# Kernel optimization log

Measured on AMD Instinct MI355X. Metric: run time of the kernel, lower is better.

Reference implementation:

```python
import jax, jax.numpy as jnp
import numpy as np

N, V, E = 65536, 2048, 1024
TEMPERATURE = 0.5
EPS = 1e-10
LOG_PARAM_Q = -2.995732273553991


def _l2_normalize(x, axis):
    # matches torch F.normalize(p=2): x / max(||x||, 1e-12)
    n = jnp.sqrt(jnp.sum(x * x, axis=axis, keepdims=True))
    return x / jnp.maximum(n, 1e-12)


def setup_inputs() -> dict:
    key = jax.random.key(0)
    k1, k2, k3 = jax.random.split(key, 3)
    z = jax.random.normal(k1, (N, E), dtype=jnp.float32)
    emb_weight = jax.random.normal(k2, (V, E), dtype=jnp.float32)
    U = jax.random.uniform(k3, (N, V), dtype=jnp.float32)
    return {"z": z, "emb_weight": emb_weight, "U": U}


def reference(z, emb_weight, U):
    kappa_q = jnp.exp(jnp.float32(LOG_PARAM_Q)) + jnp.float32(1.0)
    zn = _l2_normalize(z, axis=1)              # [N, E]
    emb = _l2_normalize(emb_weight, axis=1)    # [V, E]
    # logit = -distances = kappa_q * z @ emb.T
    logit = kappa_q * jnp.matmul(zn, emb.T)    # [N, V]
    # gumbel-softmax sample (training branch)
    g = -jnp.log(-jnp.log(U + EPS) + EPS)
    tokens = jax.nn.softmax((logit + g) / TEMPERATURE, axis=-1)  # [N, V]
    z_q = jnp.matmul(tokens, emb)              # [N, E]
    return (tokens, z_q)
```

## Files before the change

kernel.cpp:

```cpp
#include <hip/hip_runtime.h>
#include <hip/hip_bf16.h>
#include <stdint.h>

typedef short bf16x8 __attribute__((ext_vector_type(8)));
typedef float floatx4 __attribute__((ext_vector_type(4)));

#define N_ROWS 65536
#define V_DIM 2048
#define E_DIM 1024

__device__ __forceinline__ short f2bf(float x) {
  union { float f; uint32_t u; } c; c.f = x;
  uint32_t r = (c.u + 0x7FFFu + ((c.u >> 16) & 1u)) >> 16;
  return (short)(uint16_t)r;
}
__device__ __forceinline__ float bf16f(short b) {
  union { uint32_t u; float f; } c; c.u = ((uint32_t)(uint16_t)b) << 16;
  return c.f;
}

__device__ __forceinline__ float wave_sum(float v) {
#pragma unroll
  for (int o = 32; o > 0; o >>= 1) v += __shfl_xor(v, o);
  return v;
}
__device__ __forceinline__ float wave_max(float v) {
#pragma unroll
  for (int o = 32; o > 0; o >>= 1) v = fmaxf(v, __shfl_xor(v, o));
  return v;
}

__device__ __forceinline__ void gll16(const short* g, short* l) {
  __builtin_amdgcn_global_load_lds(
      (const __attribute__((address_space(1))) void*)g,
      (__attribute__((address_space(3))) void*)l, 16, 0, 0);
}

#define FRAG(base, R, c) \
  (*(const bf16x8*)((const char*)(base) + ((R) << 7) + (((((c) >> 3) ^ ((R) & 7))) << 4)))

__global__ __launch_bounds__(256) void k_norm_emb(const float* __restrict__ W,
                                                  short* __restrict__ embn,
                                                  short* __restrict__ embnT) {
  const int v = blockIdx.x;
  const int t = threadIdx.x;
  const int w = t >> 6, l = t & 63;
  const float4 val = *(const float4*)&W[(size_t)v * E_DIM + t * 4];
  float ss = val.x * val.x + val.y * val.y + val.z * val.z + val.w * val.w;
  ss = wave_sum(ss);
  __shared__ float red[4];
  if (l == 0) red[w] = ss;
  __syncthreads();
  ss = red[0] + red[1] + red[2] + red[3];
  const float inv = 1.0f / fmaxf(sqrtf(ss), 1e-12f);
  short4 o;
  o.x = f2bf(val.x * inv);
  o.y = f2bf(val.y * inv);
  o.z = f2bf(val.z * inv);
  o.w = f2bf(val.w * inv);
  *(short4*)&embn[(size_t)v * E_DIM + t * 4] = o;
  embnT[(size_t)(t * 4 + 0) * V_DIM + v] = o.x;
  embnT[(size_t)(t * 4 + 1) * V_DIM + v] = o.y;
  embnT[(size_t)(t * 4 + 2) * V_DIM + v] = o.z;
  embnT[(size_t)(t * 4 + 3) * V_DIM + v] = o.w;
}

__global__ __launch_bounds__(256) void k_norm_z(const float* __restrict__ Z,
                                                short* __restrict__ zn) {
  const int w = threadIdx.x >> 6, l = threadIdx.x & 63;
  const int row = blockIdx.x * 4 + w;
  const float* zr = Z + (size_t)row * E_DIM;
  float4 v[4];
  float ss = 0.f;
#pragma unroll
  for (int i = 0; i < 4; ++i) {
    v[i] = *(const float4*)&zr[(i * 64 + l) * 4];
    ss += v[i].x * v[i].x + v[i].y * v[i].y + v[i].z * v[i].z + v[i].w * v[i].w;
  }
  ss = wave_sum(ss);
  const float SCALE = 2.0f * (expf(-2.995732273553991f) + 1.0f);
  const float inv = SCALE / fmaxf(sqrtf(ss), 1e-12f);
  short* zo = zn + (size_t)row * E_DIM;
#pragma unroll
  for (int i = 0; i < 4; ++i) {
    short4 o;
    o.x = f2bf(v[i].x * inv);
    o.y = f2bf(v[i].y * inv);
    o.z = f2bf(v[i].z * inv);
    o.w = f2bf(v[i].w * inv);
    *(short4*)&zo[(i * 64 + l) * 4] = o;
  }
}

template <int KDIM, int NBX, int EPI>
__global__ __launch_bounds__(512, 2) void k_gemm8(
    const short* __restrict__ A, const short* __restrict__ B,
    const float* __restrict__ U, short* __restrict__ Pb,
    float* __restrict__ partials, const float* __restrict__ invsum,
    float* __restrict__ C, int cpx) {
  __shared__ __align__(16) short Sm[65536];
  const int NT = KDIM / 32;
  const int tid = threadIdx.x;
  const int wv = tid >> 6, lane = tid & 63;
  const int lr = lane & 15, lh = lane >> 4;
  const int wr = wv >> 2, wc = wv & 3;
  const int d = blockIdx.x;
  const int L = (d & 7) * cpx + (d >> 3);
  const int by = L / NBX, bx = L % NBX;
  const int m0 = by * 256, n0 = bx * 256;
  const int sg = (((lane & 3) ^ ((lane >> 2) & 3) ^ ((lane >> 4) & 3)) << 3);
  const int srow = wv * 16 + (lane >> 2);
  const short* gA = A + (size_t)(m0 + srow) * KDIM + sg;
  const short* gB = B + (size_t)(n0 + srow) * KDIM + sg;
  const int fslot = lh ^ ((lr ^ (lr >> 2)) & 3);
  const int aoff = wr * 8192 + lr * 64 + fslot * 16;
  const int boff = wc * 4096 + lr * 64 + fslot * 16;

#pragma unroll
  for (int t = 0; t < 2; ++t) {
#pragma unroll
    for (int q = 0; q < 2; ++q) {
      gll16(gA + (size_t)(q * 128) * KDIM + t * 32, Sm + t * 8192 + q * 4096 + wv * 512);
      gll16(gB + (size_t)(q * 128) * KDIM + t * 32, Sm + 32768 + t * 8192 + q * 4096 + wv * 512);
    }
  }
  asm volatile("s_waitcnt vmcnt(4)" ::: "memory");
  __builtin_amdgcn_s_barrier();
  __builtin_amdgcn_sched_barrier(0);

  floatx4 acc[8][4] = {};

#define DO_TILE(KT, STAGE)                                                          \
  {                                                                                 \
    const int cb_ = (KT) & 3;                                                       \
    const char* Ab_ = (const char*)Sm + cb_ * 16384;                                \
    const char* Bb_ = (const char*)Sm + 65536 + cb_ * 16384;                        \
    short* An_ = Sm + (((KT) + 2) & 3) * 8192;                                      \
    short* Bn_ = Sm + 32768 + (((KT) + 2) & 3) * 8192;                              \
    const size_t kc_ = (size_t)((KT) + 2) * 32;                                     \
    bf16x8 bfr[4], af[4];                                                           \
    _Pragma("unroll")                                                               \
    for (int n = 0; n < 4; ++n) bfr[n] = *(const bf16x8*)(Bb_ + boff + n * 1024);   \
    _Pragma("unroll")                                                               \
    for (int i = 0; i < 4; ++i) af[i] = *(const bf16x8*)(Ab_ + aoff + i * 1024);    \
    if (STAGE) {                                                                    \
      _Pragma("unroll")                                                             \
      for (int q = 0; q < 2; ++q) {                                                 \
        gll16(gA + (size_t)(q * 128) * KDIM + kc_, An_ + q * 4096 + wv * 512);      \
        gll16(gB + (size_t)(q * 128) * KDIM + kc_, Bn_ + q * 4096 + wv * 512);      \
      }                                                                             \
    }                                                                               \
    __builtin_amdgcn_s_setprio(1);                                                  \
    _Pragma("unroll")                                                               \
    for (int i = 0; i < 4; ++i) {                                                   \
      _Pragma("unroll")                                                             \
      for (int n = 0; n < 4; ++n)                                                   \
        acc[i][n] =                                                                 \
            __builtin_amdgcn_mfma_f32_16x16x32_bf16(af[i], bfr[n], acc[i][n], 0, 0, 0); \
    }                                                                               \
    __builtin_amdgcn_s_setprio(0);                                                  \
    _Pragma("unroll")                                                               \
    for (int i = 0; i < 4; ++i)                                                     \
      af[i] = *(const bf16x8*)(Ab_ + aoff + 4096 + i * 1024);                       \
    __builtin_amdgcn_s_setprio(1);                                                  \
    _Pragma("unroll")                                                               \
    for (int i = 0; i < 4; ++i) {                                                   \
      _Pragma("unroll")                                                             \
      for (int n = 0; n < 4; ++n)                                                   \
        acc[4 + i][n] =                                                             \
            __builtin_amdgcn_mfma_f32_16x16x32_bf16(af[i], bfr[n], acc[4 + i][n], 0, 0, 0); \
    }                                                                               \
    __builtin_amdgcn_s_setprio(0);                                                  \
    if (STAGE) { asm volatile("s_waitcnt vmcnt(4)" ::: "memory"); }                 \
    else       { asm volatile("s_waitcnt vmcnt(0)" ::: "memory"); }                 \
    __builtin_amdgcn_s_barrier();                                                   \
    __builtin_amdgcn_sched_barrier(0);                                              \
  }

  for (int kt = 0; kt < NT - 2; ++kt) DO_TILE(kt, 1);
  DO_TILE(NT - 2, 0);
  DO_TILE(NT - 1, 0);
#undef DO_TILE

  const int gr0 = m0 + wr * 128 + lh * 4;
  const int gc0 = n0 + wc * 64 + lr;
  if (EPI == 0) {
    float rs[8][4] = {};
#pragma unroll
    for (int m = 0; m < 8; ++m)
#pragma unroll
      for (int n = 0; n < 4; ++n) {
        const int col = gc0 + n * 16;
#pragma unroll
        for (int j = 0; j < 4; ++j) {
          const int row = gr0 + m * 16 + j;
          const size_t idx = (size_t)row * V_DIM + col;
          const float u = U[idx];
          const float e = __expf(acc[m][n][j] - 2.f * __logf(-__logf(u + 1e-10f) + 1e-10f));
          const short eb = f2bf(e);
          Pb[idx] = eb;
          rs[m][j] += bf16f(eb);
        }
      }
#pragma unroll
    for (int m = 0; m < 8; ++m)
#pragma unroll
      for (int j = 0; j < 4; ++j) {
        float s = rs[m][j];
        s += __shfl_xor(s, 1); s += __shfl_xor(s, 2);
        s += __shfl_xor(s, 4); s += __shfl_xor(s, 8);
        if (lr == 0)
          partials[(size_t)(gr0 + m * 16 + j) * 32 + bx * 4 + wc] = s;
      }
  } else {
#pragma unroll
    for (int m = 0; m < 8; ++m)
#pragma unroll
      for (int j = 0; j < 4; ++j) {
        const int row = gr0 + m * 16 + j;
        const float s = invsum[row];
#pragma unroll
        for (int n = 0; n < 4; ++n)
          C[(size_t)row * E_DIM + gc0 + n * 16] = acc[m][n][j] * s;
      }
  }
}

__global__ __launch_bounds__(256) void k_rowsum_inv(const float* __restrict__ partials,
                                                    float* __restrict__ invsum) {
  const int r = blockIdx.x * 256 + threadIdx.x;
  const float4* p = (const float4*)&partials[(size_t)r * 32];
  float s = 0.f;
#pragma unroll
  for (int i = 0; i < 8; ++i) { float4 v = p[i]; s += v.x + v.y + v.z + v.w; }
  invsum[r] = 1.f / s;
}

__global__ __launch_bounds__(256) void k_token_norm(const short* __restrict__ Pb,
                                                    const float* __restrict__ invsum,
                                                    float* __restrict__ tokens) {
  const size_t stride = (size_t)gridDim.x * 256 * 8;
  for (size_t i = ((size_t)blockIdx.x * 256 + threadIdx.x) * 8;
       i < (size_t)N_ROWS * V_DIM; i += stride) {
    const float s = invsum[i >> 11];
    const bf16x8 v = *(const bf16x8*)&Pb[i];
    float4 o0, o1;
    o0.x = bf16f(v[0]) * s; o0.y = bf16f(v[1]) * s;
    o0.z = bf16f(v[2]) * s; o0.w = bf16f(v[3]) * s;
    o1.x = bf16f(v[4]) * s; o1.y = bf16f(v[5]) * s;
    o1.z = bf16f(v[6]) * s; o1.w = bf16f(v[7]) * s;
    *(float4*)&tokens[i] = o0;
    *(float4*)&tokens[i + 4] = o1;
  }
}

__global__ __launch_bounds__(256) void k_gemm_nt(const short* __restrict__ A,
                                                 const short* __restrict__ B,
                                                 float* __restrict__ C,
                                                 int lda, int ldb, int ldc, int K) {
  __shared__ __align__(16) short As[128][64];
  __shared__ __align__(16) short Bs[128][64];
  const int t = threadIdx.x;
  const int w = t >> 6, l = t & 63;
  const int lr = l & 15, lh = l >> 4;
  const int m0 = blockIdx.y * 128, n0 = blockIdx.x * 128;
  const int wm = (w >> 1) * 64, wn = (w & 1) * 64;
  floatx4 acc[4][4] = {};
  for (int k0 = 0; k0 < K; k0 += 64) {
    __syncthreads();
#pragma unroll
    for (int i = 0; i < 4; ++i) {
      const int c = i * 256 + t;
      const int r = c >> 3, c8 = (c & 7) * 8;
      *(bf16x8*)&As[r][c8] = *(const bf16x8*)&A[(size_t)(m0 + r) * lda + k0 + c8];
      *(bf16x8*)&Bs[r][c8] = *(const bf16x8*)&B[(size_t)(n0 + r) * ldb + k0 + c8];
    }
    __syncthreads();
#pragma unroll
    for (int kk = 0; kk < 64; kk += 32) {
      bf16x8 af[4], bfr[4];
#pragma unroll
      for (int m = 0; m < 4; ++m) af[m] = *(const bf16x8*)&As[wm + m * 16 + lr][kk + lh * 8];
#pragma unroll
      for (int n = 0; n < 4; ++n) bfr[n] = *(const bf16x8*)&Bs[wn + n * 16 + lr][kk + lh * 8];
#pragma unroll
      for (int m = 0; m < 4; ++m)
#pragma unroll
        for (int n = 0; n < 4; ++n)
          acc[m][n] = __builtin_amdgcn_mfma_f32_16x16x32_bf16(af[m], bfr[n], acc[m][n], 0, 0, 0);
    }
  }
#pragma unroll
  for (int m = 0; m < 4; ++m)
#pragma unroll
    for (int n = 0; n < 4; ++n) {
      const int col = n0 + wn + n * 16 + lr;
#pragma unroll
      for (int j = 0; j < 4; ++j)
        C[(size_t)(m0 + wm + m * 16 + lh * 4 + j) * ldc + col] = acc[m][n][j];
    }
}

__global__ __launch_bounds__(256) void k_gemm_nt_f32a(const float* __restrict__ A,
                                                      const short* __restrict__ B,
                                                      float* __restrict__ C,
                                                      int lda, int ldb, int ldc, int K) {
  __shared__ __align__(16) short As[128][64];
  __shared__ __align__(16) short Bs[128][64];
  const int t = threadIdx.x;
  const int w = t >> 6, l = t & 63;
  const int lr = l & 15, lh = l >> 4;
  const int m0 = blockIdx.y * 128, n0 = blockIdx.x * 128;
  const int wm = (w >> 1) * 64, wn = (w & 1) * 64;
  floatx4 acc[4][4] = {};
  for (int k0 = 0; k0 < K; k0 += 64) {
    __syncthreads();
#pragma unroll
    for (int i = 0; i < 4; ++i) {
      const int c = i * 256 + t;
      const int r = c >> 3, c8 = (c & 7) * 8;
      const float4 a0 = *(const float4*)&A[(size_t)(m0 + r) * lda + k0 + c8];
      const float4 a1 = *(const float4*)&A[(size_t)(m0 + r) * lda + k0 + c8 + 4];
      bf16x8 va;
      va[0] = f2bf(a0.x); va[1] = f2bf(a0.y); va[2] = f2bf(a0.z); va[3] = f2bf(a0.w);
      va[4] = f2bf(a1.x); va[5] = f2bf(a1.y); va[6] = f2bf(a1.z); va[7] = f2bf(a1.w);
      *(bf16x8*)&As[r][c8] = va;
      *(bf16x8*)&Bs[r][c8] = *(const bf16x8*)&B[(size_t)(n0 + r) * ldb + k0 + c8];
    }
    __syncthreads();
#pragma unroll
    for (int kk = 0; kk < 64; kk += 32) {
      bf16x8 af[4], bfr[4];
#pragma unroll
      for (int m = 0; m < 4; ++m) af[m] = *(const bf16x8*)&As[wm + m * 16 + lr][kk + lh * 8];
#pragma unroll
      for (int n = 0; n < 4; ++n) bfr[n] = *(const bf16x8*)&Bs[wn + n * 16 + lr][kk + lh * 8];
#pragma unroll
      for (int m = 0; m < 4; ++m)
#pragma unroll
        for (int n = 0; n < 4; ++n)
          acc[m][n] = __builtin_amdgcn_mfma_f32_16x16x32_bf16(af[m], bfr[n], acc[m][n], 0, 0, 0);
    }
  }
#pragma unroll
  for (int m = 0; m < 4; ++m)
#pragma unroll
    for (int n = 0; n < 4; ++n) {
      const int col = n0 + wn + n * 16 + lr;
#pragma unroll
      for (int j = 0; j < 4; ++j)
        C[(size_t)(m0 + wm + m * 16 + lh * 4 + j) * ldc + col] = acc[m][n][j];
    }
}

__global__ __launch_bounds__(256) void k_gumbel_softmax(float* __restrict__ S,
                                                        const float* __restrict__ U) {
  const int t = threadIdx.x;
  const int w = t >> 6, l = t & 63;
  const size_t base = (size_t)blockIdx.x * V_DIM + t * 8;
  const float4 s0 = *(const float4*)&S[base];
  const float4 s1 = *(const float4*)&S[base + 4];
  const float4 u0 = *(const float4*)&U[base];
  const float4 u1 = *(const float4*)&U[base + 4];
  float x[8];
  x[0] = s0.x - 2.f * __logf(-__logf(u0.x + 1e-10f) + 1e-10f);
  x[1] = s0.y - 2.f * __logf(-__logf(u0.y + 1e-10f) + 1e-10f);
  x[2] = s0.z - 2.f * __logf(-__logf(u0.z + 1e-10f) + 1e-10f);
  x[3] = s0.w - 2.f * __logf(-__logf(u0.w + 1e-10f) + 1e-10f);
  x[4] = s1.x - 2.f * __logf(-__logf(u1.x + 1e-10f) + 1e-10f);
  x[5] = s1.y - 2.f * __logf(-__logf(u1.y + 1e-10f) + 1e-10f);
  x[6] = s1.z - 2.f * __logf(-__logf(u1.z + 1e-10f) + 1e-10f);
  x[7] = s1.w - 2.f * __logf(-__logf(u1.w + 1e-10f) + 1e-10f);
  float lm = x[0];
#pragma unroll
  for (int i = 1; i < 8; ++i) lm = fmaxf(lm, x[i]);
  lm = wave_max(lm);
  __shared__ float redA[4], redB[4];
  if (l == 0) redA[w] = lm;
  __syncthreads();
  const float m = fmaxf(fmaxf(redA[0], redA[1]), fmaxf(redA[2], redA[3]));
  float p[8];
  float ls = 0.f;
#pragma unroll
  for (int i = 0; i < 8; ++i) { p[i] = __expf(x[i] - m); ls += p[i]; }
  ls = wave_sum(ls);
  if (l == 0) redB[w] = ls;
  __syncthreads();
  const float inv = 1.0f / (redB[0] + redB[1] + redB[2] + redB[3]);
  float4 o0 = make_float4(p[0] * inv, p[1] * inv, p[2] * inv, p[3] * inv);
  float4 o1 = make_float4(p[4] * inv, p[5] * inv, p[6] * inv, p[7] * inv);
  *(float4*)&S[base] = o0;
  *(float4*)&S[base + 4] = o1;
}

extern "C" void kernel_launch(void* const* d_in, const int* in_sizes, int n_in,
                              void* d_out, int out_size, void* d_ws, size_t ws_size,
                              hipStream_t stream) {
  const float* z = (const float*)d_in[0];
  const float* W = (const float*)d_in[1];
  const float* U = (const float*)d_in[2];
  float* tokens = (float*)d_out;
  float* zq = tokens + (size_t)N_ROWS * V_DIM;
  short* zn = (short*)zq;

  short* embn = (short*)d_ws;
  short* embnT = embn + (size_t)V_DIM * E_DIM;

  const size_t NEED = (size_t)V_DIM * E_DIM * 2 * 2
                    + (size_t)N_ROWS * 32 * 4
                    + (size_t)N_ROWS * 4
                    + (size_t)N_ROWS * V_DIM * 2;

  k_norm_emb<<<V_DIM, 256, 0, stream>>>(W, embn, embnT);
  k_norm_z<<<N_ROWS / 4, 256, 0, stream>>>(z, zn);

  if (ws_size >= NEED) {
    float* partials = (float*)(embnT + (size_t)V_DIM * E_DIM);
    float* invsum = partials + (size_t)N_ROWS * 32;
    short* Pb = (short*)(invsum + N_ROWS);
    k_gemm8<E_DIM, 8, 0><<<2048, 512, 0, stream>>>(
        zn, embn, U, Pb, partials, nullptr, nullptr, 2048 / 8);
    k_rowsum_inv<<<N_ROWS / 256, 256, 0, stream>>>(partials, invsum);
    k_token_norm<<<2048, 256, 0, stream>>>(Pb, invsum, tokens);
    k_gemm8<V_DIM, 4, 1><<<1024, 512, 0, stream>>>(
        Pb, embnT, nullptr, nullptr, nullptr, invsum, zq, 1024 / 8);
  } else {
    k_gemm_nt<<<dim3(V_DIM / 128, N_ROWS / 128), 256, 0, stream>>>(
        zn, embn, tokens, E_DIM, E_DIM, V_DIM, E_DIM);
    k_gumbel_softmax<<<N_ROWS, 256, 0, stream>>>(tokens, U);
    k_gemm_nt_f32a<<<dim3(E_DIM / 128, N_ROWS / 128), 256, 0, stream>>>(
        tokens, embnT, zq, V_DIM, V_DIM, E_DIM, V_DIM);
  }
}
```

Before: 1.004 ms.

## Switch GEMM LDS pipeline from 4-stage prefetch-2 to double buffering

The GEMM main loop moves from a 4-slot shared-memory ring with two tiles in flight to a 2-slot double buffer that prefetches only the next tile and waits for all loads each iteration. This halves LDS use per block (64KB instead of 128KB), which may allow more blocks per CU or relieve LDS pressure. The cost is less load latency hiding, since each iteration fully drains outstanding global loads before its barrier.

After: 1.063 ms. 1.06x slower.

```diff
diff --git a/kernel.cpp b/kernel.cpp
--- a/kernel.cpp
+++ b/kernel.cpp
@@ -98,7 +98,7 @@
     const float* __restrict__ U, short* __restrict__ Pb,
     float* __restrict__ partials, const float* __restrict__ invsum,
     float* __restrict__ C, int cpx) {
-  __shared__ __align__(16) short Sm[65536];
+  __shared__ __align__(16) short Sm[32768];
   const int NT = KDIM / 32;
   const int tid = threadIdx.x;
   const int wv = tid >> 6, lane = tid & 63;
@@ -116,47 +116,35 @@
   const int aoff = wr * 8192 + lr * 64 + fslot * 16;
   const int boff = wc * 4096 + lr * 64 + fslot * 16;
 
-#pragma unroll
-  for (int t = 0; t < 2; ++t) {
-#pragma unroll
-    for (int q = 0; q < 2; ++q) {
-      gll16(gA + (size_t)(q * 128) * KDIM + t * 32, Sm + t * 8192 + q * 4096 + wv * 512);
-      gll16(gB + (size_t)(q * 128) * KDIM + t * 32, Sm + 32768 + t * 8192 + q * 4096 + wv * 512);
-    }
-  }
-  asm volatile("s_waitcnt vmcnt(4)" ::: "memory");
-  __builtin_amdgcn_s_barrier();
-  __builtin_amdgcn_sched_barrier(0);
-
   floatx4 acc[8][4] = {};
 
-#define DO_TILE(KT, STAGE)                                                          \
+#define STAGE(KT)                                                                   \
   {                                                                                 \
-    const int cb_ = (KT) & 3;                                                       \
-    const char* Ab_ = (const char*)Sm + cb_ * 16384;                                \
-    const char* Bb_ = (const char*)Sm + 65536 + cb_ * 16384;                        \
-    short* An_ = Sm + (((KT) + 2) & 3) * 8192;                                      \
-    short* Bn_ = Sm + 32768 + (((KT) + 2) & 3) * 8192;                              \
-    const size_t kc_ = (size_t)((KT) + 2) * 32;                                     \
+    short* An_ = Sm + ((KT) & 1) * 8192;                                            \
+    short* Bn_ = Sm + 16384 + ((KT) & 1) * 8192;                                    \
+    const size_t kc_ = (size_t)(KT) * 32;                                           \
+    gll16(gA + kc_, An_ + wv * 512);                                                \
+    gll16(gA + (size_t)128 * KDIM + kc_, An_ + 4096 + wv * 512);                    \
+    gll16(gB + kc_, Bn_ + wv * 512);                                                \
+    gll16(gB + (size_t)128 * KDIM + kc_, Bn_ + 4096 + wv * 512);                    \
+  }
+
+#define DO_TILE(KT, STG)                                                            \
+  {                                                                                 \
+    const char* Ab_ = (const char*)Sm + ((KT) & 1) * 16384;                         \
+    const char* Bb_ = (const char*)Sm + 32768 + ((KT) & 1) * 16384;                 \
     bf16x8 bfr[4], af[4];                                                           \
     _Pragma("unroll")                                                               \
     for (int n = 0; n < 4; ++n) bfr[n] = *(const bf16x8*)(Bb_ + boff + n * 1024);   \
     _Pragma("unroll")                                                               \
     for (int i = 0; i < 4; ++i) af[i] = *(const bf16x8*)(Ab_ + aoff + i * 1024);    \
-    if (STAGE) {                                                                    \
-      _Pragma("unroll")                                                             \
-      for (int q = 0; q < 2; ++q) {                                                 \
-        gll16(gA + (size_t)(q * 128) * KDIM + kc_, An_ + q * 4096 + wv * 512);      \
-        gll16(gB + (size_t)(q * 128) * KDIM + kc_, Bn_ + q * 4096 + wv * 512);      \
-      }                                                                             \
-    }                                                                               \
+    if (STG) STAGE((KT) + 1);                                                       \
     __builtin_amdgcn_s_setprio(1);                                                  \
     _Pragma("unroll")                                                               \
     for (int i = 0; i < 4; ++i) {                                                   \
       _Pragma("unroll")                                                             \
       for (int n = 0; n < 4; ++n)                                                   \
-        acc[i][n] =                                                                 \
-            __builtin_amdgcn_mfma_f32_16x16x32_bf16(af[i], bfr[n], acc[i][n], 0, 0, 0); \
+        acc[i][n] = __builtin_amdgcn_mfma_f32_16x16x32_bf16(af[i], bfr[n], acc[i][n], 0, 0, 0); \
     }                                                                               \
     __builtin_amdgcn_s_setprio(0);                                                  \
     _Pragma("unroll")                                                               \
@@ -167,19 +155,25 @@
     for (int i = 0; i < 4; ++i) {                                                   \
       _Pragma("unroll")                                                             \
       for (int n = 0; n < 4; ++n)                                                   \
-        acc[4 + i][n] =                                                             \
-            __builtin_amdgcn_mfma_f32_16x16x32_bf16(af[i], bfr[n], acc[4 + i][n], 0, 0, 0); \
+        acc[4 + i][n] = __builtin_amdgcn_mfma_f32_16x16x32_bf16(af[i], bfr[n], acc[4 + i][n], 0, 0, 0); \
     }                                                                               \
     __builtin_amdgcn_s_setprio(0);                                                  \
-    if (STAGE) { asm volatile("s_waitcnt vmcnt(4)" ::: "memory"); }                 \
-    else       { asm volatile("s_waitcnt vmcnt(0)" ::: "memory"); }                 \
-    __builtin_amdgcn_s_barrier();                                                   \
-    __builtin_amdgcn_sched_barrier(0);                                              \
-  }
-
-  for (int kt = 0; kt < NT - 2; ++kt) DO_TILE(kt, 1);
-  DO_TILE(NT - 2, 0);
+    if (STG) {                                                                      \
+      asm volatile("s_waitcnt vmcnt(0)" ::: "memory");                              \
+      __builtin_amdgcn_s_barrier();                                                 \
+      __builtin_amdgcn_sched_barrier(0);                                            \
+    }                                                                               \
+  }
+
+  STAGE(0);
+  asm volatile("s_waitcnt vmcnt(0)" ::: "memory");
+  __builtin_amdgcn_s_barrier();
+  __builtin_amdgcn_sched_barrier(0);
+
+#pragma unroll 2
+  for (int kt = 0; kt < NT - 1; ++kt) DO_TILE(kt, 1);
   DO_TILE(NT - 1, 0);
+#undef STAGE
 #undef DO_TILE
 
   const int gr0 = m0 + wr * 128 + lh * 4;
```
